# Kernel tuning notes

Hardware: AMD Instinct MI355X
Metric: run time of the kernel (lower is better)

## Reference

```python
import jax, jax.numpy as jnp
import numpy as np

HEADS = 8

def _layernorm(x, g, b, eps=1e-5):
    mu = x.mean(-1, keepdims=True)
    var = ((x - mu) ** 2).mean(-1, keepdims=True)
    return (x - mu) * jax.lax.rsqrt(var + eps) * g + b

def _four_region_attention(x, ln_g, ln_b, w_qkv, b_qkv, w_out, b_out):
    b, n, dim = x.shape
    W = int(np.sqrt(n))  # H == W, n = H*W
    xn = _layernorm(x, ln_g, ln_b)
    qkv = xn @ w_qkv + b_qkv  # [b, n, 3*inner]
    q, k, v = jnp.split(qkv, 3, axis=-1)
    split_heads = lambda t: t.reshape(b, n, HEADS, -1).transpose(0, 2, 1, 3)  # b h n d
    q, k, v = map(split_heads, (q, k, v))
    dh = q.shape[-1]
    scale = dh ** -0.5
    scores = jnp.einsum('bhqd,bhkd->bhqk', q, k) * scale  # [b, h, n, n]
    # region masks: query pos (h,w), key pos (i,j); to_qkv is position-wise
    # linear so per-region K/V recompute == slicing global K/V.
    row = jnp.arange(n) // W
    col = jnp.arange(n) % W
    le_r = row[None, :] <= row[:, None]  # i <= h
    ge_r = row[None, :] >= row[:, None]  # i >= h
    le_c = col[None, :] <= col[:, None]  # j <= w
    ge_c = col[None, :] >= col[:, None]  # j >= w
    masks = (le_r & le_c, le_r & ge_c, ge_r & le_c, ge_r & ge_c)
    neg = jnp.finfo(scores.dtype).min
    acc = jnp.zeros_like(q)
    for m in masks:  # all 4 regions are always non-empty (contain (h,w))
        attn = jax.nn.softmax(jnp.where(m, scores, neg), axis=-1)
        attn = jax.nn.relu(attn)  # identity on softmax output; kept for fidelity
        acc = acc + jnp.einsum('bhqk,bhkd->bhqd', attn, v)
    out = (acc / 4.0).transpose(0, 2, 1, 3).reshape(b, n, HEADS * dh)
    return out @ w_out + b_out

def setup_inputs() -> dict:
    key = jax.random.key(0)
    ks = jax.random.split(key, 3)
    b, n, dim = 8, 1024, 512
    dim_head = 64
    inner = HEADS * dim_head
    s = lambda fan: 1.0 / np.sqrt(fan)
    return {
        'x': jax.random.normal(ks[0], (b, n, dim), jnp.float32),
        'ln_g': jnp.ones((dim,), jnp.float32),
        'ln_b': jnp.zeros((dim,), jnp.float32),
        'w_qkv': jax.random.normal(ks[1], (dim, 3 * inner), jnp.float32) * s(dim),
        'b_qkv': jnp.zeros((3 * inner,), jnp.float32),
        'w_out': jax.random.normal(ks[2], (inner, dim), jnp.float32) * s(inner),
        'b_out': jnp.zeros((dim,), jnp.float32),
    }

def reference(x, ln_g, ln_b, w_qkv, b_qkv, w_out, b_out):
    return _four_region_attention(x, ln_g, ln_b, w_qkv, b_qkv, w_out, b_out)
```

## Files before the change

kernel.cpp:

```cpp
#include <hip/hip_runtime.h>
#include <hip/hip_bf16.h>

typedef unsigned short ushort_t;
typedef unsigned int uint32;
typedef __attribute__((ext_vector_type(8))) short short8;
typedef __attribute__((ext_vector_type(4))) float f32x4;
typedef __attribute__((ext_vector_type(16))) float f32x16;

#define BATCH 8
#define SEQ 1024
#define DIM 512
#define NHEADS 8
#define DH 64
#define NQKV 1536

__device__ __forceinline__ float bf2f(ushort_t u){ return __uint_as_float(((uint32)u) << 16); }
__device__ __forceinline__ ushort_t f2bf(float f){
  uint32 u = __float_as_uint(f);
  return (ushort_t)((u + 0x7fffu + ((u >> 16) & 1u)) >> 16);
}
__device__ __forceinline__ short8 ld8(const ushort_t* p){ return *reinterpret_cast<const short8*>(p); }
__device__ __forceinline__ f32x4 mfma16(short8 a, short8 b, f32x4 c){
  return __builtin_amdgcn_mfma_f32_16x16x32_bf16(a, b, c, 0, 0, 0);
}
__device__ __forceinline__ f32x16 mfma32(short8 a, short8 b, f32x16 c){
  return __builtin_amdgcn_mfma_f32_32x32x16_bf16(a, b, c, 0, 0, 0);
}
__device__ __forceinline__ void async16(const ushort_t* g, ushort_t* l){
  __builtin_amdgcn_global_load_lds((const __attribute__((address_space(1))) void*)g,
                                   (__attribute__((address_space(3))) void*)l, 16, 0, 0);
}
__device__ __forceinline__ uint32 cvtpk_bf16(float lo, float hi){
  uint32 d;
  asm("v_cvt_pk_bf16_f32 %0, %1, %2" : "=v"(d) : "v"(lo), "v"(hi));
  return d;
}
__device__ __forceinline__ void permswap32(uint32& a, uint32& b){
  asm volatile("v_permlane32_swap_b32 %0, %1" : "+v"(a), "+v"(b));
}
__device__ __forceinline__ short8 mk8(uint32 a, uint32 b, uint32 c, uint32 d){
  union { uint32 u[4]; short8 v; } t;
  t.u[0] = a; t.u[1] = b; t.u[2] = c; t.u[3] = d; return t.v;
}

__global__ __launch_bounds__(256) void prep_kernel(const float* __restrict__ x,
                                                   const float* __restrict__ g,
                                                   const float* __restrict__ bt,
                                                   ushort_t* __restrict__ xn,
                                                   const float* __restrict__ wqkv,
                                                   ushort_t* __restrict__ wqkvT,
                                                   const float* __restrict__ wout,
                                                   ushort_t* __restrict__ woutT){
  __shared__ float t[32][33];
  int bid = blockIdx.x;
  if (bid < 2048){
    int row  = bid * 4 + (threadIdx.x >> 6);
    int lane = threadIdx.x & 63;
    const float* xr = x + (size_t)row * DIM + lane * 8;
    float4 d0 = *reinterpret_cast<const float4*>(xr);
    float4 d1 = *reinterpret_cast<const float4*>(xr + 4);
    float v[8] = {d0.x, d0.y, d0.z, d0.w, d1.x, d1.y, d1.z, d1.w};
    float s = 0.f, ss = 0.f;
    #pragma unroll
    for (int i = 0; i < 8; i++){ s += v[i]; ss += v[i] * v[i]; }
    #pragma unroll
    for (int off = 1; off < 64; off <<= 1){ s += __shfl_xor(s, off); ss += __shfl_xor(ss, off); }
    float mean = s * (1.0f / DIM);
    float var  = ss * (1.0f / DIM) - mean * mean;
    float rstd = rsqrtf(fmaxf(var, 0.f) + 1e-5f);
    float4 g0 = *reinterpret_cast<const float4*>(g  + lane * 8);
    float4 g1 = *reinterpret_cast<const float4*>(g  + lane * 8 + 4);
    float4 b0 = *reinterpret_cast<const float4*>(bt + lane * 8);
    float4 b1 = *reinterpret_cast<const float4*>(bt + lane * 8 + 4);
    float gv[8] = {g0.x, g0.y, g0.z, g0.w, g1.x, g1.y, g1.z, g1.w};
    float bv[8] = {b0.x, b0.y, b0.z, b0.w, b1.x, b1.y, b1.z, b1.w};
    ushort_t o[8];
    #pragma unroll
    for (int i = 0; i < 8; i++) o[i] = f2bf((v[i] - mean) * rstd * gv[i] + bv[i]);
    uint4 od;
    od.x = o[0] | ((uint32)o[1] << 16); od.y = o[2] | ((uint32)o[3] << 16);
    od.z = o[4] | ((uint32)o[5] << 16); od.w = o[6] | ((uint32)o[7] << 16);
    *reinterpret_cast<uint4*>(xn + (size_t)row * DIM + lane * 8) = od;
  } else {
    const float* in; ushort_t* out; int R, C, bx, by;
    if (bid < 2816){ int b = bid - 2048; in = wqkv; out = wqkvT; R = 512; C = 1536; bx = b % 48; by = b / 48; }
    else           { int b = bid - 2816; in = wout; out = woutT; R = 512; C = 512;  bx = b % 16; by = b / 16; }
    int tx = threadIdx.x & 31, ty = threadIdx.x >> 5;
    int r0 = by * 32, c0 = bx * 32;
    #pragma unroll
    for (int i = 0; i < 4; i++) t[ty + 8*i][tx] = in[(size_t)(r0 + ty + 8*i) * C + c0 + tx];
    __syncthreads();
    #pragma unroll
    for (int i = 0; i < 4; i++) out[(size_t)(c0 + ty + 8*i) * R + r0 + tx] = f2bf(t[tx][ty + 8*i]);
  }
}

template<int MT>
__device__ __forceinline__ void gemm_core_t(const ushort_t* __restrict__ A,
                                            const ushort_t* __restrict__ Bt,
                                            int m0, int n0,
                                            ushort_t* ldsA, ushort_t* ldsB,
                                            f32x4 acc[MT][4]){
  int tid = threadIdx.x, w = tid >> 6, lane = tid & 63;
  int c16 = lane & 15, quad = lane >> 4;
  int r8 = lane >> 3, p8 = lane & 7;
  int srcChunk = p8 ^ r8;
  int w_row = w >> 1, w_col = w & 1;

  const ushort_t* ga[MT]; const ushort_t* gb[4];
  #pragma unroll
  for (int c = 0; c < MT; c++)
    ga[c] = A  + (size_t)(m0 + c * 32 + w * 8 + r8) * DIM + srcChunk * 8;
  #pragma unroll
  for (int c = 0; c < 4; c++)
    gb[c] = Bt + (size_t)(n0 + c * 32 + w * 8 + r8) * DIM + srcChunk * 8;
  #pragma unroll
  for (int mt = 0; mt < MT; mt++)
    #pragma unroll
    for (int nt = 0; nt < 4; nt++) acc[mt][nt] = (f32x4){0.f, 0.f, 0.f, 0.f};

  for (int it = 0; it < 8; it++){
    #pragma unroll
    for (int c = 0; c < MT; c++){ async16(ga[c], &ldsA[(c * 32 + w * 8) * 64]); ga[c] += 64; }
    #pragma unroll
    for (int c = 0; c < 4;  c++){ async16(gb[c], &ldsB[(c * 32 + w * 8) * 64]); gb[c] += 64; }
    __syncthreads();
    #pragma unroll
    for (int kk = 0; kk < 2; kk++){
      short8 af[MT], bfr[4];
      int phys = ((kk * 4 + quad) ^ (c16 & 7)) * 8;
      #pragma unroll
      for (int mt = 0; mt < MT; mt++)
        af[mt] = ld8(&ldsA[(w_row * (MT * 16) + mt * 16 + c16) * 64 + phys]);
      #pragma unroll
      for (int nt = 0; nt < 4; nt++)
        bfr[nt] = ld8(&ldsB[(w_col * 64 + nt * 16 + c16) * 64 + phys]);
      #pragma unroll
      for (int mt = 0; mt < MT; mt++)
        #pragma unroll
        for (int nt = 0; nt < 4; nt++)
          acc[mt][nt] = mfma16(af[mt], bfr[nt], acc[mt][nt]);
    }
    __syncthreads();
  }
}

__global__ __launch_bounds__(256) void qkv_gemm_kernel(const ushort_t* __restrict__ xn,
                                                       const ushort_t* __restrict__ wT,
                                                       const float* __restrict__ bias,
                                                       ushort_t* __restrict__ Qo,
                                                       ushort_t* __restrict__ Ko,
                                                       ushort_t* __restrict__ Vt){
  __shared__ __align__(16) ushort_t ldsA[64 * 64];
  __shared__ __align__(16) ushort_t ldsB[128 * 64];
  int m0 = blockIdx.x * 64, n0 = blockIdx.y * 128;
  f32x4 acc[2][4];
  gemm_core_t<2>(xn, wT, m0, n0, ldsA, ldsB, acc);

  int lane = threadIdx.x & 63, w = threadIdx.x >> 6;
  int c16 = lane & 15, quad = lane >> 4;
  int w_row = w >> 1, w_col = w & 1;
  int region = n0 >> 9;

  if (region < 2){
    float sc = (region == 0) ? 0.18033688011112042f : 1.0f;
    #pragma unroll
    for (int nt = 0; nt < 4; nt++){
      int col = n0 + w_col * 64 + nt * 16 + c16;
      float bv = bias[col];
      int cr = col & 511, h = cr >> 6, dd = cr & 63;
      #pragma unroll
      for (int mt = 0; mt < 2; mt++){
        #pragma unroll
        for (int r = 0; r < 4; r++){
          int row = m0 + w_row * 32 + mt * 16 + quad * 4 + r;
          int b = row >> 10, n = row & 1023;
          ushort_t o = f2bf((acc[mt][nt][r] + bv) * sc);
          if (region == 0) Qo[(((size_t)(b * NHEADS + h)) * SEQ + n) * DH + dd] = o;
          else             Ko[(((size_t)(b * NHEADS + h)) * SEQ + n) * DH + dd] = o;
        }
      }
    }
  } else {
    #pragma unroll
    for (int nt = 0; nt < 4; nt++){
      int col = n0 + w_col * 64 + nt * 16 + c16;
      float bv = bias[col];
      int c2 = col - 1024; int h = c2 >> 6, dd = c2 & 63;
      #pragma unroll
      for (int mt = 0; mt < 2; mt++){
        int row0 = m0 + w_row * 32 + mt * 16 + quad * 4;
        int b = row0 >> 10, n = row0 & 1023;
        ushort_t o[4];
        #pragma unroll
        for (int r = 0; r < 4; r++) o[r] = f2bf(acc[mt][nt][r] + bv);
        uint2 val;
        val.x = o[0] | ((uint32)o[1] << 16);
        val.y = o[2] | ((uint32)o[3] << 16);
        *reinterpret_cast<uint2*>(Vt + (((size_t)(b * NHEADS + h)) * 128 + (n >> 3)) * 512
                                  + dd * 8 + (n & 7)) = val;
      }
    }
  }
}

__global__ __launch_bounds__(256) void out_gemm_kernel(const ushort_t* __restrict__ ctx,
                                                       const ushort_t* __restrict__ wT,
                                                       const float* __restrict__ bias,
                                                       float* __restrict__ out){
  __shared__ __align__(16) ushort_t ldsA[32 * 64];
  __shared__ __align__(16) ushort_t ldsB[128 * 64];
  int m0 = blockIdx.x * 32, n0 = blockIdx.y * 128;
  f32x4 acc[1][4];
  gemm_core_t<1>(ctx, wT, m0, n0, ldsA, ldsB, acc);

  int lane = threadIdx.x & 63, w = threadIdx.x >> 6;
  int c16 = lane & 15, quad = lane >> 4;
  int w_row = w >> 1, w_col = w & 1;
  #pragma unroll
  for (int nt = 0; nt < 4; nt++){
    int col = n0 + w_col * 64 + nt * 16 + c16;
    float bv = bias[col];
    #pragma unroll
    for (int r = 0; r < 4; r++){
      int row = m0 + w_row * 16 + quad * 4 + r;
      out[(size_t)row * DIM + col] = acc[0][nt][r] + bv;
    }
  }
}

__global__ __launch_bounds__(256, 2) void attn_kernel(const ushort_t* __restrict__ Qg,
                                                      const ushort_t* __restrict__ Kg,
                                                      const ushort_t* __restrict__ Vtg,
                                                      ushort_t* __restrict__ ctx){
  int bh = blockIdx.x;
  int wv = threadIdx.x >> 6, lane = threadIdx.x & 63;
  int qt = blockIdx.y * 4 + wv;
  int w  = lane & 31;
  int hi = lane >> 5;
  int hq = qt;

  const ushort_t* Qh = Qg  + (size_t)bh * SEQ * DH;
  const ushort_t* Kh = Kg  + (size_t)bh * SEQ * DH;
  const ushort_t* Vh = Vtg + (size_t)bh * SEQ * DH;

  short8 qf[4];
  {
    const ushort_t* qp = Qh + (size_t)(qt * 32 + w) * DH + hi * 8;
    #pragma unroll
    for (int f = 0; f < 4; f++) qf[f] = ld8(qp + f * 16);
  }
  const ushort_t* kp = Kh + (size_t)w * DH + hi * 8;

  float mle[16], mge[16];
  #pragma unroll
  for (int r = 0; r < 16; r++){
    int jr = (r & 3) + 8 * (r >> 2) + 4 * hi;
    mle[r] = (jr <= w) ? 1.f : 0.f;
    mge[r] = (jr >= w) ? 1.f : 0.f;
  }

  auto qk = [&](const short8* kf) -> f32x16 {
    f32x16 s;
    #pragma unroll
    for (int r = 0; r < 16; r++) s[r] = 0.f;
    #pragma unroll
    for (int f = 0; f < 4; f++) s = mfma32(kf[f], qf[f], s);
    return s;
  };

  float tle = 0.f, tge = 0.f, ble = 0.f, bge = 0.f;
  auto p1 = [&](const short8* kf, int i){
    f32x16 s = qk(kf);
    float a0 = 0.f, a1 = 0.f, g0 = 0.f, g1 = 0.f;
    #pragma unroll
    for (int r = 0; r < 16; r++){
      float e = __builtin_amdgcn_exp2f(s[r]);
      if (r & 1){ a1 = fmaf(mle[r], e, a1); g1 = fmaf(mge[r], e, g1); }
      else      { a0 = fmaf(mle[r], e, a0); g0 = fmaf(mge[r], e, g0); }
    }
    float sle = a0 + a1, sge = g0 + g1;
    if (i <= hq){ tle += sle; tge += sge; }
    if (i >= hq){ ble += sle; bge += sge; }
  };
  {
    short8 kA[4], kB[4];
    #pragma unroll
    for (int f = 0; f < 4; f++) kA[f] = ld8(kp + f * 16);
    for (int i = 0; i < 32; i += 2){
      #pragma unroll
      for (int f = 0; f < 4; f++) kB[f] = ld8(kp + (size_t)(i + 1) * 2048 + f * 16);
      p1(kA, i);
      int nx = (i + 2) & 31;
      #pragma unroll
      for (int f = 0; f < 4; f++) kA[f] = ld8(kp + (size_t)nx * 2048 + f * 16);
      p1(kB, i + 1);
    }
  }
  tle += __shfl_xor(tle, 32); tge += __shfl_xor(tge, 32);
  ble += __shfl_xor(ble, 32); bge += __shfl_xor(bge, 32);
  float i1 = 0.25f / fmaxf(tle, 1e-30f);
  float i2 = 0.25f / fmaxf(tge, 1e-30f);
  float i3 = 0.25f / fmaxf(ble, 1e-30f);
  float i4 = 0.25f / fmaxf(bge, 1e-30f);

  float wcur[16], wbt[16];
  #pragma unroll
  for (int r = 0; r < 16; r++){
    wcur[r] = fmaf(i1, mle[r], i2 * mge[r]);
    wbt[r]  = fmaf(i3, mle[r], i4 * mge[r]);
  }

  f32x16 accLo, accHi;
  #pragma unroll
  for (int r = 0; r < 16; r++){ accLo[r] = 0.f; accHi[r] = 0.f; }
  const ushort_t* vbase = Vh + (size_t)hi * 512 + (size_t)w * 8;

  auto p2 = [&](const short8* kf, int i){
    short8 vl0 = ld8(vbase + (size_t)i * 2048);
    short8 vl1 = ld8(vbase + (size_t)i * 2048 + 1024);
    short8 vh0 = ld8(vbase + (size_t)i * 2048 + 256);
    short8 vh1 = ld8(vbase + (size_t)i * 2048 + 1280);
    f32x16 s = qk(kf);
    if (i == hq){
      #pragma unroll
      for (int r = 0; r < 16; r++) wcur[r] += wbt[r];
    } else if (i == hq + 1){
      #pragma unroll
      for (int r = 0; r < 16; r++) wcur[r] = wbt[r];
    }
    float P[16];
    #pragma unroll
    for (int r = 0; r < 16; r++) P[r] = __builtin_amdgcn_exp2f(s[r]) * wcur[r];
    uint32 x0 = cvtpk_bf16(P[0],  P[1]);
    uint32 x1 = cvtpk_bf16(P[2],  P[3]);
    uint32 y0 = cvtpk_bf16(P[4],  P[5]);
    uint32 y1 = cvtpk_bf16(P[6],  P[7]);
    uint32 x2 = cvtpk_bf16(P[8],  P[9]);
    uint32 x3 = cvtpk_bf16(P[10], P[11]);
    uint32 y2 = cvtpk_bf16(P[12], P[13]);
    uint32 y3 = cvtpk_bf16(P[14], P[15]);
    permswap32(x0, y0);
    permswap32(x1, y1);
    permswap32(x2, y2);
    permswap32(x3, y3);
    short8 fa0 = mk8(x0, x1, y0, y1);
    short8 fa1 = mk8(x2, x3, y2, y3);
    accLo = mfma32(fa0, vl0, accLo);
    accLo = mfma32(fa1, vl1, accLo);
    accHi = mfma32(fa0, vh0, accHi);
    accHi = mfma32(fa1, vh1, accHi);
  };
  {
    short8 kA[4], kB[4];
    #pragma unroll
    for (int f = 0; f < 4; f++) kA[f] = ld8(kp + f * 16);
    for (int i = 0; i < 32; i += 2){
      #pragma unroll
      for (int f = 0; f < 4; f++) kB[f] = ld8(kp + (size_t)(i + 1) * 2048 + f * 16);
      p2(kA, i);
      int nx = (i + 2) & 31;
      #pragma unroll
      for (int f = 0; f < 4; f++) kA[f] = ld8(kp + (size_t)nx * 2048 + f * 16);
      p2(kB, i + 1);
    }
  }

  int bidx = bh >> 3, h = bh & 7;
  size_t obase = ((size_t)(bidx * SEQ + qt * 32)) * DIM + h * DH + w;
  #pragma unroll
  for (int r = 0; r < 16; r++){
    int qrow = (r & 3) + 8 * (r >> 2) + 4 * hi;
    ctx[obase + (size_t)qrow * DIM]      = f2bf(accLo[r]);
    ctx[obase + (size_t)qrow * DIM + 32] = f2bf(accHi[r]);
  }
}

extern "C" void kernel_launch(void* const* d_in, const int* in_sizes, int n_in,
                              void* d_out, int out_size, void* d_ws, size_t ws_size,
                              hipStream_t stream){
  (void)in_sizes; (void)n_in; (void)out_size; (void)ws_size;
  const float* x    = (const float*)d_in[0];
  const float* ln_g = (const float*)d_in[1];
  const float* ln_b = (const float*)d_in[2];
  const float* wqkv = (const float*)d_in[3];
  const float* bqkv = (const float*)d_in[4];
  const float* wout = (const float*)d_in[5];
  const float* bout = (const float*)d_in[6];
  float* out = (float*)d_out;

  char* ws = (char*)d_ws;
  ushort_t* xn    = (ushort_t*)(ws);
  ushort_t* ctx   = (ushort_t*)(ws);
  ushort_t* wqkvT = (ushort_t*)(ws + 8388608);
  ushort_t* woutT = (ushort_t*)(ws + 9961472);
  ushort_t* Qb    = (ushort_t*)(ws + 10485760);
  ushort_t* Kb    = (ushort_t*)(ws + 18874368);
  ushort_t* Vtb   = (ushort_t*)(ws + 27262976);

  hipLaunchKernelGGL(prep_kernel,     dim3(3072),    dim3(256), 0, stream,
                     x, ln_g, ln_b, xn, wqkv, wqkvT, wout, woutT);
  hipLaunchKernelGGL(qkv_gemm_kernel, dim3(128, 12), dim3(256), 0, stream, xn, wqkvT, bqkv, Qb, Kb, Vtb);
  hipLaunchKernelGGL(attn_kernel,     dim3(64, 8),   dim3(256), 0, stream, Qb, Kb, Vtb, ctx);
  hipLaunchKernelGGL(out_gemm_kernel, dim3(256, 4),  dim3(256), 0, stream, ctx, woutT, bout, out);
}
```

Measured before the change: 176.9 us.

## Split attention key range across two waves per query tile with LDS reduction

Each 32-row query tile is now handled by two waves, each covering half of the key/row range, with the softmax denominators and partial outputs combined through shared memory. The grid doubles and launch bounds ask for four blocks per CU, so more waves are available to hide latency and each wave's serial loop is half as long. In exchange it adds two block barriers, LDS traffic for the partial sums, and pressure to fit the register budget at the higher occupancy target.

```diff
diff --git a/kernel.cpp b/kernel.cpp
--- a/kernel.cpp
+++ b/kernel.cpp
@@ -229,16 +229,21 @@
   }
 }
 
-__global__ __launch_bounds__(256, 2) void attn_kernel(const ushort_t* __restrict__ Qg,
+__global__ __launch_bounds__(256, 4) void attn_kernel(const ushort_t* __restrict__ Qg,
                                                       const ushort_t* __restrict__ Kg,
                                                       const ushort_t* __restrict__ Vtg,
                                                       ushort_t* __restrict__ ctx){
+  __shared__ float sdn[2][2][32][4];
+  __shared__ float obuf[2][32][64];
+
   int bh = blockIdx.x;
   int wv = threadIdx.x >> 6, lane = threadIdx.x & 63;
-  int qt = blockIdx.y * 4 + wv;
+  int qsel = wv >> 1, half = wv & 1;
+  int qt = blockIdx.y * 2 + qsel;
   int w  = lane & 31;
   int hi = lane >> 5;
   int hq = qt;
+  int i0 = half << 4;
 
   const ushort_t* Qh = Qg  + (size_t)bh * SEQ * DH;
   const ushort_t* Kh = Kg  + (size_t)bh * SEQ * DH;
@@ -286,12 +291,13 @@
   {
     short8 kA[4], kB[4];
     #pragma unroll
-    for (int f = 0; f < 4; f++) kA[f] = ld8(kp + f * 16);
-    for (int i = 0; i < 32; i += 2){
+    for (int f = 0; f < 4; f++) kA[f] = ld8(kp + (size_t)i0 * 2048 + f * 16);
+    for (int ii = 0; ii < 16; ii += 2){
+      int i = i0 + ii;
       #pragma unroll
       for (int f = 0; f < 4; f++) kB[f] = ld8(kp + (size_t)(i + 1) * 2048 + f * 16);
       p1(kA, i);
-      int nx = (i + 2) & 31;
+      int nx = i0 + ((ii + 2) & 15);
       #pragma unroll
       for (int f = 0; f < 4; f++) kA[f] = ld8(kp + (size_t)nx * 2048 + f * 16);
       p1(kB, i + 1);
@@ -299,6 +305,15 @@
   }
   tle += __shfl_xor(tle, 32); tge += __shfl_xor(tge, 32);
   ble += __shfl_xor(ble, 32); bge += __shfl_xor(bge, 32);
+  if (lane < 32){
+    float4 d4 = {tle, tge, ble, bge};
+    *reinterpret_cast<float4*>(&sdn[qsel][half][w][0]) = d4;
+  }
+  __syncthreads();
+  {
+    float4 o4 = *reinterpret_cast<const float4*>(&sdn[qsel][1 - half][w][0]);
+    tle += o4.x; tge += o4.y; ble += o4.z; bge += o4.w;
+  }
   float i1 = 0.25f / fmaxf(tle, 1e-30f);
   float i2 = 0.25f / fmaxf(tge, 1e-30f);
   float i3 = 0.25f / fmaxf(ble, 1e-30f);
@@ -307,8 +322,9 @@
   float wcur[16], wbt[16];
   #pragma unroll
   for (int r = 0; r < 16; r++){
-    wcur[r] = fmaf(i1, mle[r], i2 * mge[r]);
-    wbt[r]  = fmaf(i3, mle[r], i4 * mge[r]);
+    float wa = fmaf(i1, mle[r], i2 * mge[r]);
+    wbt[r]   = fmaf(i3, mle[r], i4 * mge[r]);
+    wcur[r]  = (i0 <= hq) ? wa : wbt[r];
   }
 
   f32x16 accLo, accHi;
@@ -354,25 +370,39 @@
   {
     short8 kA[4], kB[4];
     #pragma unroll
-    for (int f = 0; f < 4; f++) kA[f] = ld8(kp + f * 16);
-    for (int i = 0; i < 32; i += 2){
+    for (int f = 0; f < 4; f++) kA[f] = ld8(kp + (size_t)i0 * 2048 + f * 16);
+    for (int ii = 0; ii < 16; ii += 2){
+      int i = i0 + ii;
       #pragma unroll
       for (int f = 0; f < 4; f++) kB[f] = ld8(kp + (size_t)(i + 1) * 2048 + f * 16);
       p2(kA, i);
-      int nx = (i + 2) & 31;
+      int nx = i0 + ((ii + 2) & 15);
       #pragma unroll
       for (int f = 0; f < 4; f++) kA[f] = ld8(kp + (size_t)nx * 2048 + f * 16);
       p2(kB, i + 1);
     }
   }
 
-  int bidx = bh >> 3, h = bh & 7;
-  size_t obase = ((size_t)(bidx * SEQ + qt * 32)) * DIM + h * DH + w;
-  #pragma unroll
-  for (int r = 0; r < 16; r++){
-    int qrow = (r & 3) + 8 * (r >> 2) + 4 * hi;
-    ctx[obase + (size_t)qrow * DIM]      = f2bf(accLo[r]);
-    ctx[obase + (size_t)qrow * DIM + 32] = f2bf(accHi[r]);
+  if (half){
+    #pragma unroll
+    for (int r = 0; r < 16; r++){
+      int qrow = (r & 3) + 8 * (r >> 2) + 4 * hi;
+      obuf[qsel][qrow][w]      = accLo[r];
+      obuf[qsel][qrow][w + 32] = accHi[r];
+    }
+  }
+  __syncthreads();
+  if (!half){
+    int bidx = bh >> 3, h = bh & 7;
+    size_t obase = ((size_t)(bidx * SEQ + qt * 32)) * DIM + h * DH + w;
+    #pragma unroll
+    for (int r = 0; r < 16; r++){
+      int qrow = (r & 3) + 8 * (r >> 2) + 4 * hi;
+      float lo = accLo[r] + obuf[qsel][qrow][w];
+      float hiv = accHi[r] + obuf[qsel][qrow][w + 32];
+      ctx[obase + (size_t)qrow * DIM]      = f2bf(lo);
+      ctx[obase + (size_t)qrow * DIM + 32] = f2bf(hiv);
+    }
   }
 }
 
@@ -401,6 +431,6 @@
   hipLaunchKernelGGL(prep_kernel,     dim3(3072),    dim3(256), 0, stream,
                      x, ln_g, ln_b, xn, wqkv, wqkvT, wout, woutT);
   hipLaunchKernelGGL(qkv_gemm_kernel, dim3(128, 12), dim3(256), 0, stream, xn, wqkvT, bqkv, Qb, Kb, Vtb);
-  hipLaunchKernelGGL(attn_kernel,     dim3(64, 8),   dim3(256), 0, stream, Qb, Kb, Vtb, ctx);
+  hipLaunchKernelGGL(attn_kernel,     dim3(64, 16),  dim3(256), 0, stream, Qb, Kb, Vtb, ctx);
   hipLaunchKernelGGL(out_gemm_kernel, dim3(256, 4),  dim3(256), 0, stream, ctx, woutT, bout, out);
 }
```

New measurement: 264.4 us. 49.4% more time.
